# Optimization experiments

Measured on AMD Instinct MI355X. Metric: run time of the kernel, lower is better.

## Reference

```python
import jax, jax.numpy as jnp
import numpy as np

O, EI, EQ = 1024, 512, 512      # output_size, embedding_img, embedding_q
DI, DQ = 2048, 300              # input_img, input_q
LI, LQ = 1024, 32               # video frames, question length
V, T = 32000, 20                # vocab, decode steps


def _lstm_scan(x, Wi, Wh, b):
    # x: [L, D]; torch LSTM gate order i, f, g, o
    xp = x @ Wi.T  # [L, 4H] precompute input projection
    H = Wh.shape[1]
    def step(carry, xt):
        h, c = carry
        g = xt + Wh @ h + b
        i, f, gg, o = jnp.split(g, 4)
        c = jax.nn.sigmoid(f) * c + jax.nn.sigmoid(i) * jnp.tanh(gg)
        h = jax.nn.sigmoid(o) * jnp.tanh(c)
        return (h, c), h
    z = jnp.zeros((H,), x.dtype)
    _, hs = jax.lax.scan(step, (z, z), xp)
    return hs  # [L, H]


def _bilstm(x, Wif, Whf, bf, Wib, Whb, bb):
    hf = _lstm_scan(x, Wif, Whf, bf)
    hb = _lstm_scan(x[::-1], Wib, Whb, bb)[::-1]
    return jnp.concatenate([hf, hb], axis=-1)  # [L, 2H]


def _forward(img_feats, q_feats, Wi_imgf, Wh_imgf, b_imgf, Wi_imgb, Wh_imgb, b_imgb, Wi_qf, Wh_qf, b_qf, Wi_qb, Wh_qb, b_qb, Wimg_h, Wimg_e, bimg, Wq_h, Wq_e, bq, Wmod, bmod, Wmod_img, Wmod_q, Wfus_img, Wfus_q, Wfus, bfus, Wi_dec, Wh_dec, b_dec, Wfin, bfin, t_dec):
    img_emb = _bilstm(img_feats, Wi_imgf, Wh_imgf, b_imgf, Wi_imgb, Wh_imgb, b_imgb)  # [LI, 2EI]
    q_emb = _bilstm(q_feats, Wi_qf, Wh_qf, b_qf, Wi_qb, Wh_qb, b_qb)                  # [LQ, 2EQ]
    # static (encoder) part of the Bahdanau score: Linear(O+2E,1) split into h-part and e-part
    e_img = img_emb @ Wimg_e + bimg  # [LI]
    e_q = q_emb @ Wq_e + bq          # [LQ]

    def dec_step(carry, _):
        h, c = carry  # decoder hidden/cell, [O]
        # per-frame / per-word attention (h contribution is a constant shift under softmax)
        a_img = jax.nn.softmax(jnp.dot(Wimg_h, h) + e_img)
        a_q = jax.nn.softmax(jnp.dot(Wq_h, h) + e_q)
        ctx_img = a_img @ img_emb  # [2EI]
        ctx_q = a_q @ q_emb        # [2EQ]
        # modality-level attention
        tmp = jnp.dot(Wmod, h) + bmod
        wi = jnp.tanh(tmp + jnp.dot(Wmod_img, ctx_img))
        wq = jnp.tanh(tmp + jnp.dot(Wmod_q, ctx_q))
        mw = jax.nn.softmax(jnp.stack([wi, wq]))  # [2]
        d_img = Wfus_img @ ctx_img  # [O]
        d_q = Wfus_q @ ctx_q        # [O]
        fs = jnp.tanh(Wfus @ h + bfus + mw[0] * d_img + mw[1] * d_q)  # gated fusion, [O]
        # single-step decoder LSTM
        g = Wi_dec @ fs + Wh_dec @ h + b_dec
        i, f, gg, o = jnp.split(g, 4)
        c = jax.nn.sigmoid(f) * c + jax.nn.sigmoid(i) * jnp.tanh(gg)
        h = jax.nn.sigmoid(o) * jnp.tanh(c)
        logits = Wfin @ h + bfin  # [V]
        return (h, c), logits

    z = jnp.zeros((O,), img_feats.dtype)
    _, logits = jax.lax.scan(dec_step, (z, z), None, length=t_dec)
    return logits  # [T, V]


def setup_inputs() -> dict:
    ks = jax.random.split(jax.random.key(0), 40)
    def n(k, shape, s=0.05):
        return jax.random.normal(k, shape, dtype=jnp.float32) * s
    inp = {
        "img_feats": n(ks[0], (LI, DI), 1.0),
        "q_feats": n(ks[1], (LQ, DQ), 1.0),
        "Wi_imgf": n(ks[2], (4 * EI, DI)),
        "Wh_imgf": n(ks[3], (4 * EI, EI)),
        "b_imgf": n(ks[4], (4 * EI,)),
        "Wi_imgb": n(ks[5], (4 * EI, DI)),
        "Wh_imgb": n(ks[6], (4 * EI, EI)),
        "b_imgb": n(ks[7], (4 * EI,)),
        "Wi_qf": n(ks[8], (4 * EQ, DQ)),
        "Wh_qf": n(ks[9], (4 * EQ, EQ)),
        "b_qf": n(ks[10], (4 * EQ,)),
        "Wi_qb": n(ks[11], (4 * EQ, DQ)),
        "Wh_qb": n(ks[12], (4 * EQ, EQ)),
        "b_qb": n(ks[13], (4 * EQ,)),
        "Wimg_h": n(ks[14], (O,)),
        "Wimg_e": n(ks[15], (2 * EI,)),
        "bimg": n(ks[16], ()),
        "Wq_h": n(ks[17], (O,)),
        "Wq_e": n(ks[18], (2 * EQ,)),
        "bq": n(ks[19], ()),
        "Wmod": n(ks[20], (O,)),
        "bmod": n(ks[21], ()),
        "Wmod_img": n(ks[22], (2 * EI,)),
        "Wmod_q": n(ks[23], (2 * EQ,)),
        "Wfus_img": n(ks[24], (O, 2 * EI)),
        "Wfus_q": n(ks[25], (O, 2 * EQ)),
        "Wfus": n(ks[26], (O, O)),
        "bfus": n(ks[27], (O,)),
        "Wi_dec": n(ks[28], (4 * O, O)),
        "Wh_dec": n(ks[29], (4 * O, O)),
        "b_dec": n(ks[30], (4 * O,)),
        "Wfin": n(ks[31], (V, O)),
        "bfin": n(ks[32], (V,)),
        "t_dec": T,
    }
    return inp


def reference(img_feats, q_feats, Wi_imgf, Wh_imgf, b_imgf, Wi_imgb, Wh_imgb, b_imgb, Wi_qf, Wh_qf, b_qf, Wi_qb, Wh_qb, b_qb, Wimg_h, Wimg_e, bimg, Wq_h, Wq_e, bq, Wmod, bmod, Wmod_img, Wmod_q, Wfus_img, Wfus_q, Wfus, bfus, Wi_dec, Wh_dec, b_dec, Wfin, bfin, t_dec):
    return _forward(img_feats, q_feats, Wi_imgf, Wh_imgf, b_imgf, Wi_imgb, Wh_imgb, b_imgb, Wi_qf, Wh_qf, b_qf, Wi_qb, Wh_qb, b_qb, Wimg_h, Wimg_e, bimg, Wq_h, Wq_e, bq, Wmod, bmod, Wmod_img, Wmod_q, Wfus_img, Wfus_q, Wfus, bfus, Wi_dec, Wh_dec, b_dec, Wfin, bfin, t_dec)
```

## Files before the change

### kernel.cpp

```cpp
#include <hip/hip_runtime.h>
#include <hip/hip_bf16.h>

typedef unsigned int  u32;
typedef unsigned short u16;
typedef unsigned long long u64;
typedef float f32x4 __attribute__((ext_vector_type(4)));
typedef short bf16x8 __attribute__((ext_vector_type(8)));
typedef u32 u32x4 __attribute__((ext_vector_type(4)));

#define AGENT __HIP_MEMORY_SCOPE_AGENT
__device__ inline float aloadf(const float* p){ return __hip_atomic_load(p, __ATOMIC_RELAXED, AGENT); }
__device__ inline void  astoref(float* p, float v){ __hip_atomic_store(p, v, __ATOMIC_RELAXED, AGENT); }
__device__ inline int   aloadi(const int* p){ return __hip_atomic_load(p, __ATOMIC_RELAXED, AGENT); }
__device__ inline void  astorei_rel(int* p, int v){ __hip_atomic_store(p, v, __ATOMIC_RELEASE, AGENT); }

__device__ __host__ inline u16 f2bf(float f){
  u32 u = __builtin_bit_cast(u32, f);
  u += 0x7fffu + ((u >> 16) & 1u);
  return (u16)(u >> 16);
}
__device__ inline float bflo(u32 a){ return __uint_as_float(a << 16); }
__device__ inline float bfhi(u32 a){ return __uint_as_float(a & 0xffff0000u); }

__device__ inline float sigm(float x){
  return __builtin_amdgcn_rcpf(1.f + __expf(-x));
}
__device__ inline float ftanh(float x){
  float xc = fminf(fmaxf(x, -15.f), 15.f);
  float e = __expf(2.f * xc);
  return (e - 1.f) * __builtin_amdgcn_rcpf(e + 1.f);
}

__device__ inline u32x4 poll4(const u32* addr, u32 want){
  u32x4 w;
  do {
    asm volatile("global_load_dwordx4 %0, %1, off sc0 sc1\n\ts_waitcnt vmcnt(0)"
                 : "=&v"(w) : "v"(addr) : "memory");
  } while ((w.x >> 16) != want || (w.y >> 16) != want ||
           (w.z >> 16) != want || (w.w >> 16) != want);
  return w;
}
__device__ inline void store4(u32* addr, u32x4 q){
  asm volatile("global_store_dwordx4 %0, %1, off sc0 sc1"
               :: "v"(addr), "v"(q) : "memory");
}

__device__ inline float wred_sum(float v){
#pragma unroll
  for (int m = 32; m >= 1; m >>= 1) v += __shfl_xor(v, m, 64);
  return v;
}
__device__ inline float bred_sum(float v, float* red, int tid){
  v = wred_sum(v);
  if ((tid & 63) == 0) red[tid >> 6] = v;
  __syncthreads();
  float r = red[0] + red[1] + red[2] + red[3];
  __syncthreads();
  return r;
}
__device__ inline float bred_max(float v, float* red, int tid){
#pragma unroll
  for (int m = 32; m >= 1; m >>= 1) v = fmaxf(v, __shfl_xor(v, m, 64));
  if ((tid & 63) == 0) red[tid >> 6] = v;
  __syncthreads();
  float r = fmaxf(fmaxf(red[0], red[1]), fmaxf(red[2], red[3]));
  __syncthreads();
  return r;
}

__device__ inline float dot1024(const u16* __restrict__ row, const float* h, int lane){
  float s = 0.f;
#pragma unroll
  for (int c = 0; c < 4; ++c){
    int e = 4 * lane + 256 * c;
    uint2 a = *(const uint2*)(row + e);
    float4 x = *(const float4*)(h + e);
    s = fmaf(bflo(a.x), x.x, s); s = fmaf(bfhi(a.x), x.y, s);
    s = fmaf(bflo(a.y), x.z, s); s = fmaf(bfhi(a.y), x.w, s);
  }
  return s;
}

__device__ inline float4 dot4(const u16* __restrict__ W, size_t r, size_t rs,
                              const float* h, int lane){
  const u16* p0 = W + (r         ) * 1024;
  const u16* p1 = W + (r + rs    ) * 1024;
  const u16* p2 = W + (r + 2 * rs) * 1024;
  const u16* p3 = W + (r + 3 * rs) * 1024;
  float s0 = 0, s1 = 0, s2 = 0, s3 = 0;
#pragma unroll
  for (int c = 0; c < 4; ++c){
    int e = 4 * lane + 256 * c;
    float4 x = *(const float4*)(h + e);
    uint2 a0 = *(const uint2*)(p0 + e);
    uint2 a1 = *(const uint2*)(p1 + e);
    uint2 a2 = *(const uint2*)(p2 + e);
    uint2 a3 = *(const uint2*)(p3 + e);
    s0 = fmaf(bflo(a0.x), x.x, s0); s0 = fmaf(bfhi(a0.x), x.y, s0);
    s0 = fmaf(bflo(a0.y), x.z, s0); s0 = fmaf(bfhi(a0.y), x.w, s0);
    s1 = fmaf(bflo(a1.x), x.x, s1); s1 = fmaf(bfhi(a1.x), x.y, s1);
    s1 = fmaf(bflo(a1.y), x.z, s1); s1 = fmaf(bfhi(a1.y), x.w, s1);
    s2 = fmaf(bflo(a2.x), x.x, s2); s2 = fmaf(bfhi(a2.x), x.y, s2);
    s2 = fmaf(bflo(a2.y), x.z, s2); s2 = fmaf(bfhi(a2.y), x.w, s2);
    s3 = fmaf(bflo(a3.x), x.x, s3); s3 = fmaf(bfhi(a3.x), x.y, s3);
    s3 = fmaf(bflo(a3.y), x.z, s3); s3 = fmaf(bfhi(a3.y), x.w, s3);
  }
  s0 = wred_sum(s0); s1 = wred_sum(s1); s2 = wred_sum(s2); s3 = wred_sum(s3);
  return make_float4(s0, s1, s2, s3);
}

__global__ void k_cvt(const float* __restrict__ s, u16* __restrict__ d, int n4){
  int i = blockIdx.x * 256 + threadIdx.x;
  int stride = gridDim.x * 256;
  const float4* s4 = (const float4*)s;
  for (; i < n4; i += stride){
    float4 v = s4[i];
    ushort4 o;
    o.x = f2bf(v.x); o.y = f2bf(v.y); o.z = f2bf(v.z); o.w = f2bf(v.w);
    ((ushort4*)d)[i] = o;
  }
}

__global__ __launch_bounds__(256, 1) void k_gemm_xp(
    const u16* __restrict__ A,
    const u16* __restrict__ B0, const u16* __restrict__ B1,
    const float* __restrict__ bias0, const float* __restrict__ bias1,
    float* __restrict__ C0, float* __restrict__ C1)
{
  const int K = 2048, N = 2048;
  const int bx = blockIdx.x, by = blockIdx.y, z = blockIdx.z;
  const u16* B = z ? B1 : B0;
  const float* bias = z ? bias1 : bias0;
  float* C = z ? C1 : C0;
  const int tid = threadIdx.x;
  const int lane = tid & 63, wv = tid >> 6;
  const int m0 = by * 128, n0 = bx * 128;
  const int wm = (wv >> 1) * 64, wn = (wv & 1) * 64;

  __shared__ __align__(16) u16 lA[128 * 32];
  __shared__ __align__(16) u16 lB[128 * 32];

  f32x4 acc[4][4];
#pragma unroll
  for (int i = 0; i < 4; ++i)
#pragma unroll
    for (int j = 0; j < 4; ++j) acc[i][j] = (f32x4){0.f, 0.f, 0.f, 0.f};

  const int lrow = tid >> 2;
  const int lcol = (tid & 3) * 8;
  const u16* aBase = A + (size_t)(m0 + lrow) * K + lcol;
  const u16* bBase = B + (size_t)(n0 + lrow) * K + lcol;

  for (int kk = 0; kk < K; kk += 32){
#pragma unroll
    for (int io = 0; io < 2; ++io){
      __builtin_amdgcn_global_load_lds(
        (const __attribute__((address_space(1))) void*)(aBase + (size_t)io * 64 * K + kk),
        (__attribute__((address_space(3))) void*)((char*)lA + wv * 1024 + io * 4096), 16, 0, 0);
      __builtin_amdgcn_global_load_lds(
        (const __attribute__((address_space(1))) void*)(bBase + (size_t)io * 64 * K + kk),
        (__attribute__((address_space(3))) void*)((char*)lB + wv * 1024 + io * 4096), 16, 0, 0);
    }
    asm volatile("s_waitcnt vmcnt(0)");
    __syncthreads();

    bf16x8 af[4], bfr[4];
#pragma unroll
    for (int i = 0; i < 4; ++i){
      af[i]  = *(const bf16x8*)&lA[(wm + i * 16 + (lane & 15)) * 32 + (lane >> 4) * 8];
      bfr[i] = *(const bf16x8*)&lB[(wn + i * 16 + (lane & 15)) * 32 + (lane >> 4) * 8];
    }
#pragma unroll
    for (int i = 0; i < 4; ++i)
#pragma unroll
      for (int j = 0; j < 4; ++j)
        acc[i][j] = __builtin_amdgcn_mfma_f32_16x16x32_bf16(af[i], bfr[j], acc[i][j], 0, 0, 0);
    __syncthreads();
  }

  const int rbase = (lane >> 4) * 4;
  const int ccol = lane & 15;
#pragma unroll
  for (int i = 0; i < 4; ++i)
#pragma unroll
    for (int j = 0; j < 4; ++j){
      int col = n0 + wn + j * 16 + ccol;
      float bv = bias[col];
#pragma unroll
      for (int r2 = 0; r2 < 4; ++r2){
        int row = m0 + wm + i * 16 + rbase + r2;
        C[(size_t)row * N + col] = acc[i][j][r2] + bv;
      }
    }
}

__global__ __launch_bounds__(256, 1) void k_qxp(
    const float* __restrict__ qf,
    const float* __restrict__ W0, const float* __restrict__ W1,
    const float* __restrict__ bb0, const float* __restrict__ bb1,
    float* __restrict__ o0, float* __restrict__ o1)
{
  const int bx = blockIdx.x;
  const int z = blockIdx.y;
  const float* W = z ? W1 : W0;
  const float* bb = z ? bb1 : bb0;
  float* o = z ? o1 : o0;
  const int tid = threadIdx.x;
  __shared__ float xs[32 * 301];
  __shared__ float Ws[64 * 301];
  for (int idx = tid; idx < 32 * 300; idx += 256){
    int m = idx / 300, k = idx - m * 300;
    xs[m * 301 + k] = qf[idx];
  }
  for (int idx = tid; idx < 64 * 300; idx += 256){
    int j = idx / 300, k = idx - j * 300;
    Ws[j * 301 + k] = W[(size_t)(bx * 64 + j) * 300 + k];
  }
  __syncthreads();
  for (int i = 0; i < 8; ++i){
    int idx = tid + i * 256;
    int nl = idx >> 5, m = idx & 31;
    float s = 0;
    for (int k = 0; k < 300; ++k) s = fmaf(xs[m * 301 + k], Ws[nl * 301 + k], s);
    o[(size_t)m * 2048 + bx * 64 + nl] = s + bb[bx * 64 + nl];
  }
}

__global__ __launch_bounds__(256, 1) void k_scan(
    const float* __restrict__ WhA, const float* __restrict__ WhB,
    const float* __restrict__ WhC, const float* __restrict__ WhD,
    const float* __restrict__ xpA, const float* __restrict__ xpB,
    const float* __restrict__ xpC, const float* __restrict__ xpD,
    float* __restrict__ emb, float* __restrict__ embT,
    float* __restrict__ qemb, float* __restrict__ qembT,
    u32* hcomm )
{
  const int tid = threadIdx.x;
  const int dir = blockIdx.x >> 5;
  const int sub = blockIdx.x & 31;
  const float* Wh = dir == 0 ? WhA : dir == 1 ? WhB : dir == 2 ? WhC : WhD;
  const float* xp = dir == 0 ? xpA : dir == 1 ? xpB : dir == 2 ? xpC : xpD;
  const int L = (dir < 2) ? 1024 : 32;
  const int rev = dir & 1;
  float* oe  = (dir < 2) ? emb  : qemb;
  float* oeT = (dir < 2) ? embT : qembT;
  const int colbase = rev ? 512 : 0;
  const int eTL = (dir < 2) ? 1024 : 32;
  const int hbase = sub * 16;
  const int lane = tid & 63, wv = tid >> 6;
  const int g = tid >> 4;
  const int seg = tid & 15;
  const bool pub = (seg == 0);

  __shared__ float hl[512];

  int grows[4];
#pragma unroll
  for (int gate = 0; gate < 4; ++gate) grows[gate] = gate * 512 + hbase + g;

  u32 wpk0[16], wpk1[16], wpk2[16], wpk3[16];
  {
    const float2* r0 = (const float2*)(Wh + (size_t)grows[0] * 512) + seg;
    const float2* r1 = (const float2*)(Wh + (size_t)grows[1] * 512) + seg;
    const float2* r2 = (const float2*)(Wh + (size_t)grows[2] * 512) + seg;
    const float2* r3 = (const float2*)(Wh + (size_t)grows[3] * 512) + seg;
#pragma unroll
    for (int i = 0; i < 16; ++i){
      float2 a0 = r0[16 * i], a1 = r1[16 * i], a2 = r2[16 * i], a3 = r3[16 * i];
      wpk0[i] = (u32)f2bf(a0.x) | ((u32)f2bf(a0.y) << 16);
      wpk1[i] = (u32)f2bf(a1.x) | ((u32)f2bf(a1.y) << 16);
      wpk2[i] = (u32)f2bf(a2.x) | ((u32)f2bf(a2.y) << 16);
      wpk3[i] = (u32)f2bf(a3.x) | ((u32)f2bf(a3.y) << 16);
    }
  }

  float creg = 0.f;
  float xpv[4] = {0.f, 0.f, 0.f, 0.f};
  if (pub){
    int t0 = rev ? (L - 1) : 0;
#pragma unroll
    for (int gate = 0; gate < 4; ++gate) xpv[gate] = xp[(size_t)t0 * 2048 + grows[gate]];
  }

  u32* hcd = hcomm + dir * 1024;

  for (int t = 0; t < L; ++t){
    const u32 want = (u32)t;
    if (tid < 128){
      u32x4 w = poll4(hcd + ((t & 1) << 9) + 4 * tid, want);
      *(float4*)&hl[4 * tid] = make_float4(bflo(w.x), bflo(w.y), bflo(w.z), bflo(w.w));
    }
    __syncthreads();

    float2 hreg[16];
#pragma unroll
    for (int i = 0; i < 16; ++i) hreg[i] = *(const float2*)&hl[2 * (seg + 16 * i)];
    float s0 = 0, s1 = 0, s2 = 0, s3 = 0;
#pragma unroll
    for (int i = 0; i < 16; ++i){
      float hx = hreg[i].x, hy = hreg[i].y;
      s0 = fmaf(bflo(wpk0[i]), hx, s0); s0 = fmaf(bfhi(wpk0[i]), hy, s0);
      s1 = fmaf(bflo(wpk1[i]), hx, s1); s1 = fmaf(bfhi(wpk1[i]), hy, s1);
      s2 = fmaf(bflo(wpk2[i]), hx, s2); s2 = fmaf(bfhi(wpk2[i]), hy, s2);
      s3 = fmaf(bflo(wpk3[i]), hx, s3); s3 = fmaf(bfhi(wpk3[i]), hy, s3);
    }
#pragma unroll
    for (int m = 1; m < 16; m <<= 1){
      s0 += __shfl_xor(s0, m, 64); s1 += __shfl_xor(s1, m, 64);
      s2 += __shfl_xor(s2, m, 64); s3 += __shfl_xor(s3, m, 64);
    }
    u32 tg = 0;
    float hout = 0.f;
    if (pub){
      float gi = s0 + xpv[0], gf = s1 + xpv[1], gg = s2 + xpv[2], go = s3 + xpv[3];
      creg = sigm(gf) * creg + sigm(gi) * ftanh(gg);
      hout = sigm(go) * ftanh(creg);
      tg = ((u32)(t + 1) << 16) | (u32)f2bf(hout);
    }
    u32 q0 = __shfl(tg, 0), q1 = __shfl(tg, 16), q2 = __shfl(tg, 32), q3 = __shfl(tg, 48);
    if (lane == 0)
      store4(hcd + (((t + 1) & 1) << 9) + hbase + 4 * wv, (u32x4){q0, q1, q2, q3});
    if (pub){
      const int trow = rev ? (L - 1 - t) : t;
      int col = colbase + hbase + g;
      oe[(size_t)trow * 1024 + col] = hout;
      oeT[(size_t)col * eTL + trow] = hout;
      if (t + 1 < L){
        int tn = rev ? (L - 2 - t) : (t + 1);
#pragma unroll
        for (int gate = 0; gate < 4; ++gate) xpv[gate] = xp[(size_t)tn * 2048 + grows[gate]];
      }
    }
  }
}

#define DG 64
__device__ inline void dbar(int* st, int b, int pc, int tid){
  __syncthreads();
  if (tid == 0) astorei_rel(&st[b], pc);
  if (tid < DG){
    while (aloadi(&st[tid]) < pc) {}
  }
  __syncthreads();
}

struct DecArgs {
  const float *emb, *embT, *qemb, *qembT;
  const float *Wimg_e, *bimg, *Wmod_img;
  const float *Wq_e, *bq, *Wmod_q;
  const float *Wmod, *bmod;
  const u16 *Wfus_bf; const float *bfus;
  const u16 *WfusI_bf, *WfusQ_bf;
  const u16 *Wid_bf, *Whd_bf; const float *b_dec;
  float *e_img, *m_img, *e_q, *m_q;
  float *a_img, *a_q, *ctx_img, *ctx_q;
  float *d_img, *d_q, *scal;
  u32 *tfs, *thdec;
  float *hall;
  int *st; int T;
};

__global__ __launch_bounds__(256, 1) void k_dec(DecArgs A)
{
  const int b = blockIdx.x, tid = threadIdx.x;
  const int lane = tid & 63, wv = tid >> 6;
  __shared__ __align__(16) float hl[1024];
  __shared__ __align__(16) float fsl[1024];
  __shared__ float red[4];
  __shared__ float gb[4][16];
  __shared__ float cdec[16];
  __shared__ float aql[32];
  int pc = 0;

  {
#pragma unroll
    for (int rr = 0; rr < 4; ++rr){
      int l = b * 16 + wv * 4 + rr;
      const float* er = A.emb + (size_t)l * 1024;
      float se = 0, sm = 0;
#pragma unroll
      for (int i = 0; i < 16; ++i){
        int k = lane + (i << 6);
        float x = er[k];
        se = fmaf(x, A.Wimg_e[k], se);
        sm = fmaf(x, A.Wmod_img[k], sm);
      }
      se = wred_sum(se); sm = wred_sum(sm);
      if (lane == 0){ astoref(A.e_img + l, se + A.bimg[0]); astoref(A.m_img + l, sm); }
    }
    if (b < 32 && wv == 0){
      const float* qr = A.qemb + (size_t)b * 1024;
      float se2 = 0, sm2 = 0;
#pragma unroll
      for (int i = 0; i < 16; ++i){
        int k = lane + (i << 6);
        float x = qr[k];
        se2 = fmaf(x, A.Wq_e[k], se2);
        sm2 = fmaf(x, A.Wmod_q[k], sm2);
      }
      se2 = wred_sum(se2); sm2 = wred_sum(sm2);
      if (lane == 0){ astoref(A.e_q + b, se2 + A.bq[0]); astoref(A.m_q + b, sm2); }
    }
  }
  pc++; dbar(A.st, b, pc, tid);

  if (b == 0){
    for (int k = tid; k < 1024; k += 256){ fsl[k] = aloadf(A.e_img + k); hl[k] = aloadf(A.m_img + k); }
    __syncthreads();
    float lm = -3.4e38f;
    for (int k = tid; k < 1024; k += 256) lm = fmaxf(lm, fsl[k]);
    float M = bred_max(lm, red, tid);
    float ls = 0, lw = 0;
    for (int k = tid; k < 1024; k += 256){
      float e = expf(fsl[k] - M);
      fsl[k] = e; ls += e; lw += e * hl[k];
    }
    float S = bred_sum(ls, red, tid);
    float W = bred_sum(lw, red, tid);
    float inv = 1.f / S;
    for (int k = tid; k < 1024; k += 256) astoref(A.a_img + k, fsl[k] * inv);
    if (tid == 0) astoref(A.scal + 2, W * inv);
    if (tid < 64){
      float ev = (lane < 32) ? aloadf(A.e_q + lane) : -3.4e38f;
      float mv = (lane < 32) ? aloadf(A.m_q + lane) : 0.f;
      float M2 = ev;
#pragma unroll
      for (int m = 32; m >= 1; m >>= 1) M2 = fmaxf(M2, __shfl_xor(M2, m, 64));
      float e = (lane < 32) ? expf(ev - M2) : 0.f;
      float S2 = wred_sum(e);
      float W2 = wred_sum(e * mv);
      if (lane < 32) astoref(A.a_q + lane, e / S2);
      if (lane == 0) astoref(A.scal + 3, W2 / S2);
    }
  }
  pc++; dbar(A.st, b, pc, tid);

  {
    for (int k = tid; k < 1024; k += 256) hl[k] = aloadf(A.a_img + k);
    if (tid < 32) aql[tid] = aloadf(A.a_q + tid);
    __syncthreads();
#pragma unroll
    for (int cc = 0; cc < 4; ++cc){
      int c = b * 16 + wv * 4 + cc;
      const float* eT = A.embT + (size_t)c * 1024;
      float s = 0;
#pragma unroll
      for (int i = 0; i < 16; ++i){ int l = lane + (i << 6); s = fmaf(hl[l], eT[l], s); }
      s = wred_sum(s);
      if (lane == 0) astoref(A.ctx_img + c, s);
      const float* qT = A.qembT + (size_t)c * 32;
      float sq = (lane < 32) ? aql[lane] * qT[lane] : 0.f;
      sq = wred_sum(sq);
      if (lane == 0) astoref(A.ctx_q + c, sq);
    }
  }
  pc++; dbar(A.st, b, pc, tid);

  for (int k = tid; k < 1024; k += 256){ hl[k] = aloadf(A.ctx_img + k); fsl[k] = aloadf(A.ctx_q + k); }
  __syncthreads();
  {
    int r = b * 16 + wv * 4;
    float4 si = dot4(A.WfusI_bf, (size_t)r, 1, hl, lane);
    float4 sq = dot4(A.WfusQ_bf, (size_t)r, 1, fsl, lane);
    if (lane == 0){
      astoref(A.d_img + r + 0, si.x); astoref(A.d_q + r + 0, sq.x);
      astoref(A.d_img + r + 1, si.y); astoref(A.d_q + r + 1, sq.y);
      astoref(A.d_img + r + 2, si.z); astoref(A.d_q + r + 2, sq.z);
      astoref(A.d_img + r + 3, si.w); astoref(A.d_q + r + 3, sq.w);
    }
  }
  pc++; dbar(A.st, b, pc, tid);

  const int fr = b * 16 + wv * 4;
  float dimg_r[4], dq_r[4], bfus_r[4];
#pragma unroll
  for (int rr = 0; rr < 4; ++rr){
    dimg_r[rr] = aloadf(A.d_img + fr + rr);
    dq_r[rr]   = aloadf(A.d_q + fr + rr);
    bfus_r[rr] = A.bfus[fr + rr];
  }
  const float sc2 = aloadf(A.scal + 2), sc3 = aloadf(A.scal + 3);
  const float bmod0 = A.bmod[0];
  float wmod_r[4];
#pragma unroll
  for (int i = 0; i < 4; ++i) wmod_r[i] = A.Wmod[tid + (i << 8)];

  for (int k = tid; k < 1024; k += 256) hl[k] = 0.f;
  if (tid < 16) cdec[tid] = 0.f;
  __syncthreads();

  for (int t = 0; t < A.T; ++t){
    const u32 want = (u32)(t + 1);

    float part = 0;
#pragma unroll
    for (int i = 0; i < 4; ++i) part = fmaf(wmod_r[i], hl[tid + (i << 8)], part);
    float tmp = bred_sum(part, red, tid) + bmod0;
    float wi_ = ftanh(tmp + sc2), wq_ = ftanh(tmp + sc3);
    float mx = fmaxf(wi_, wq_);
    float e0 = __expf(wi_ - mx), e1 = __expf(wq_ - mx);
    float inv01 = __builtin_amdgcn_rcpf(e0 + e1);
    float mw0 = e0 * inv01, mw1 = e1 * inv01;

    {
      float4 sf = dot4(A.Wfus_bf, (size_t)fr, 1, hl, lane);
      if (lane == 0){
        float v0 = ftanh(sf.x + bfus_r[0] + mw0 * dimg_r[0] + mw1 * dq_r[0]);
        float v1 = ftanh(sf.y + bfus_r[1] + mw0 * dimg_r[1] + mw1 * dq_r[1]);
        float v2 = ftanh(sf.z + bfus_r[2] + mw0 * dimg_r[2] + mw1 * dq_r[2]);
        float v3 = ftanh(sf.w + bfus_r[3] + mw0 * dimg_r[3] + mw1 * dq_r[3]);
        u32x4 q = { (want << 16) | (u32)f2bf(v0), (want << 16) | (u32)f2bf(v1),
                    (want << 16) | (u32)f2bf(v2), (want << 16) | (u32)f2bf(v3) };
        store4(A.tfs + fr, q);
      }
    }

    {
      u32x4 w = poll4(A.tfs + 4 * tid, want);
      *(float4*)&fsl[4 * tid] = make_float4(bflo(w.x), bflo(w.y), bflo(w.z), bflo(w.w));
    }
    __syncthreads();

    {
      size_t g0 = (size_t)wv * 1024 + b * 16;
#pragma unroll
      for (int q4 = 0; q4 < 4; ++q4){
        float4 sa = dot4(A.Wid_bf, g0 + q4 * 4, 1, fsl, lane);
        float4 sb = dot4(A.Whd_bf, g0 + q4 * 4, 1, hl,  lane);
        if (lane == 0){
          gb[wv][q4 * 4 + 0] = sa.x + sb.x + A.b_dec[g0 + q4 * 4 + 0];
          gb[wv][q4 * 4 + 1] = sa.y + sb.y + A.b_dec[g0 + q4 * 4 + 1];
          gb[wv][q4 * 4 + 2] = sa.z + sb.z + A.b_dec[g0 + q4 * 4 + 2];
          gb[wv][q4 * 4 + 3] = sa.w + sb.w + A.b_dec[g0 + q4 * 4 + 3];
        }
      }
    }
    __syncthreads();
    u32 tg = 0;
    if (tid < 16){
      float gi = gb[0][tid], gf = gb[1][tid], gg = gb[2][tid], go = gb[3][tid];
      float c = sigm(gf) * cdec[tid] + sigm(gi) * ftanh(gg);
      cdec[tid] = c;
      float h = sigm(go) * ftanh(c);
      tg = (want << 16) | (u32)f2bf(h);
      A.hall[(size_t)t * 1024 + b * 16 + tid] = h;
    }
    if (wv == 0){
      u32 q0 = __shfl(tg, 4 * lane + 0), q1 = __shfl(tg, 4 * lane + 1);
      u32 q2 = __shfl(tg, 4 * lane + 2), q3 = __shfl(tg, 4 * lane + 3);
      if (lane < 4) store4(A.thdec + b * 16 + 4 * lane, (u32x4){q0, q1, q2, q3});
    }
    {
      u32x4 w = poll4(A.thdec + 4 * tid, want);
      *(float4*)&hl[4 * tid] = make_float4(bflo(w.x), bflo(w.y), bflo(w.z), bflo(w.w));
    }
    __syncthreads();
  }
}

__global__ __launch_bounds__(256, 1) void k_logits(
    const u16* __restrict__ Wfin, const float* __restrict__ bfin,
    const float* __restrict__ hall, float* __restrict__ out, int T)
{
  __shared__ u32 hp[20 * 512];
  const int tid = threadIdx.x;
  const int lane = tid & 63, wv = tid >> 6;
  const int n2 = T * 512;
  for (int idx = tid; idx < n2; idx += 256){
    float2 v = ((const float2*)hall)[idx];
    hp[idx] = (u32)f2bf(v.x) | ((u32)f2bf(v.y) << 16);
  }
  __syncthreads();
  const int gwv = blockIdx.x * 4 + wv;
#pragma unroll
  for (int gset = 0; gset < 4; ++gset){
    int r0 = gwv * 16 + gset * 4;
    uint2 wreg[4][4];
#pragma unroll
    for (int rr = 0; rr < 4; ++rr){
      const uint2* wr = (const uint2*)(Wfin + (size_t)(r0 + rr) * 1024);
#pragma unroll
      for (int c = 0; c < 4; ++c) wreg[rr][c] = wr[lane + 64 * c];
    }
    for (int t = 0; t < T; ++t){
      const uint2* hp2 = (const uint2*)&hp[t * 512];
      float s0 = 0, s1 = 0, s2 = 0, s3 = 0;
#pragma unroll
      for (int c = 0; c < 4; ++c){
        uint2 hw = hp2[lane + 64 * c];
        float h0 = bflo(hw.x), h1 = bfhi(hw.x), h2 = bflo(hw.y), h3 = bfhi(hw.y);
        uint2 a;
        a = wreg[0][c];
        s0 = fmaf(bflo(a.x), h0, s0); s0 = fmaf(bfhi(a.x), h1, s0);
        s0 = fmaf(bflo(a.y), h2, s0); s0 = fmaf(bfhi(a.y), h3, s0);
        a = wreg[1][c];
        s1 = fmaf(bflo(a.x), h0, s1); s1 = fmaf(bfhi(a.x), h1, s1);
        s1 = fmaf(bflo(a.y), h2, s1); s1 = fmaf(bfhi(a.y), h3, s1);
        a = wreg[2][c];
        s2 = fmaf(bflo(a.x), h0, s2); s2 = fmaf(bfhi(a.x), h1, s2);
        s2 = fmaf(bflo(a.y), h2, s2); s2 = fmaf(bfhi(a.y), h3, s2);
        a = wreg[3][c];
        s3 = fmaf(bflo(a.x), h0, s3); s3 = fmaf(bfhi(a.x), h1, s3);
        s3 = fmaf(bflo(a.y), h2, s3); s3 = fmaf(bfhi(a.y), h3, s3);
      }
      s0 = wred_sum(s0); s1 = wred_sum(s1); s2 = wred_sum(s2); s3 = wred_sum(s3);
      if (lane == 0){
        float* orow = out + (size_t)t * 32000;
        orow[r0 + 0] = s0 + bfin[r0 + 0];
        orow[r0 + 1] = s1 + bfin[r0 + 1];
        orow[r0 + 2] = s2 + bfin[r0 + 2];
        orow[r0 + 3] = s3 + bfin[r0 + 3];
      }
    }
  }
}

extern "C" void kernel_launch(void* const* d_in, const int* in_sizes, int n_in,
                              void* d_out, int out_size, void* d_ws, size_t ws_size,
                              hipStream_t stream)
{
  const float* img_feats = (const float*)d_in[0];
  const float* q_feats   = (const float*)d_in[1];
  const float* Wi_imgf = (const float*)d_in[2];
  const float* Wh_imgf = (const float*)d_in[3];
  const float* b_imgf  = (const float*)d_in[4];
  const float* Wi_imgb = (const float*)d_in[5];
  const float* Wh_imgb = (const float*)d_in[6];
  const float* b_imgb  = (const float*)d_in[7];
  const float* Wi_qf = (const float*)d_in[8];
  const float* Wh_qf = (const float*)d_in[9];
  const float* b_qf  = (const float*)d_in[10];
  const float* Wi_qb = (const float*)d_in[11];
  const float* Wh_qb = (const float*)d_in[12];
  const float* b_qb  = (const float*)d_in[13];
  const float* Wimg_e = (const float*)d_in[15];
  const float* bimg   = (const float*)d_in[16];
  const float* Wq_e   = (const float*)d_in[18];
  const float* bq     = (const float*)d_in[19];
  const float* Wmod   = (const float*)d_in[20];
  const float* bmod   = (const float*)d_in[21];
  const float* Wmod_img = (const float*)d_in[22];
  const float* Wmod_q   = (const float*)d_in[23];
  const float* Wfus_img = (const float*)d_in[24];
  const float* Wfus_q   = (const float*)d_in[25];
  const float* Wfus     = (const float*)d_in[26];
  const float* bfus     = (const float*)d_in[27];
  const float* Wi_dec = (const float*)d_in[28];
  const float* Wh_dec = (const float*)d_in[29];
  const float* b_dec  = (const float*)d_in[30];
  const float* Wfin = (const float*)d_in[31];
  const float* bfin = (const float*)d_in[32];
  const int T = out_size / 32000;

  char* ws = (char*)d_ws;
  size_t off = 0;
  auto alloc = [&](size_t bytes){ size_t o = off; off += (bytes + 255) & ~(size_t)255; return o; };
  const size_t oA    = alloc(1024ull * 2048 * 2);
  const size_t oWiF  = alloc(2048ull * 2048 * 2);
  const size_t oWiB  = alloc(2048ull * 2048 * 2);
  const size_t oWfin = alloc(32000ull * 1024 * 2);
  const size_t oWfu  = alloc(1024ull * 1024 * 2);
  const size_t oWfI  = alloc(1024ull * 1024 * 2);
  const size_t oWfQ  = alloc(1024ull * 1024 * 2);
  const size_t oWid  = alloc(4096ull * 1024 * 2);
  const size_t oWhd  = alloc(4096ull * 1024 * 2);
  const size_t oxpF  = alloc(1024ull * 2048 * 4);
  const size_t oxpB  = alloc(1024ull * 2048 * 4);
  const size_t oxpQF = alloc(32ull * 2048 * 4);
  const size_t oxpQB = alloc(32ull * 2048 * 4);
  const size_t oemb  = alloc(1024ull * 1024 * 4);
  const size_t oembT = alloc(1024ull * 1024 * 4);
  const size_t oqemb = alloc(32ull * 1024 * 4);
  const size_t oqembT= alloc(1024ull * 32 * 4);
  const size_t ohall = alloc(20ull * 1024 * 4);
  const size_t oeimg = alloc(1024 * 4);
  const size_t omimg = alloc(1024 * 4);
  const size_t oeq   = alloc(32 * 4);
  const size_t omq   = alloc(32 * 4);
  const size_t oaimg = alloc(1024 * 4);
  const size_t oaq   = alloc(32 * 4);
  const size_t octxi = alloc(1024 * 4);
  const size_t octxq = alloc(1024 * 4);
  const size_t odimg = alloc(1024 * 4);
  const size_t odq   = alloc(1024 * 4);
  const size_t oCTRL = off;
  const size_t ohcomm = alloc(4ull * 2 * 512 * 4);
  const size_t otfs   = alloc(1024 * 4);
  const size_t othdec = alloc(1024 * 4);
  const size_t odst   = alloc(64 * 4);
  const size_t oscal  = alloc(64 * 4);
  const size_t ctrlBytes = off - oCTRL;
  (void)ws_size; (void)n_in; (void)in_sizes;

  hipMemsetAsync(ws + oCTRL, 0, ctrlBytes, stream);

  auto cvt = [&](const float* s, size_t o, long n){
    int n4 = (int)(n >> 2);
    int g = (n4 + 255) / 256; if (g > 2048) g = 2048;
    k_cvt<<<dim3(g), dim3(256), 0, stream>>>(s, (u16*)(ws + o), n4);
  };
  cvt(img_feats, oA, 1024L * 2048);
  cvt(Wi_imgf, oWiF, 2048L * 2048);
  cvt(Wi_imgb, oWiB, 2048L * 2048);
  cvt(Wfin, oWfin, 32000L * 1024);
  cvt(Wfus, oWfu, 1024L * 1024);
  cvt(Wfus_img, oWfI, 1024L * 1024);
  cvt(Wfus_q, oWfQ, 1024L * 1024);
  cvt(Wi_dec, oWid, 4096L * 1024);
  cvt(Wh_dec, oWhd, 4096L * 1024);

  k_gemm_xp<<<dim3(16, 8, 2), dim3(256), 0, stream>>>(
      (const u16*)(ws + oA), (const u16*)(ws + oWiF), (const u16*)(ws + oWiB),
      b_imgf, b_imgb, (float*)(ws + oxpF), (float*)(ws + oxpB));

  k_qxp<<<dim3(32, 2), dim3(256), 0, stream>>>(
      q_feats, Wi_qf, Wi_qb, b_qf, b_qb,
      (float*)(ws + oxpQF), (float*)(ws + oxpQB));

  k_scan<<<dim3(128), dim3(256), 0, stream>>>(
      Wh_imgf, Wh_imgb, Wh_qf, Wh_qb,
      (const float*)(ws + oxpF), (const float*)(ws + oxpB),
      (const float*)(ws + oxpQF), (const float*)(ws + oxpQB),
      (float*)(ws + oemb), (float*)(ws + oembT),
      (float*)(ws + oqemb), (float*)(ws + oqembT),
      (u32*)(ws + ohcomm));

  DecArgs DA;
  DA.emb = (const float*)(ws + oemb); DA.embT = (const float*)(ws + oembT);
  DA.qemb = (const float*)(ws + oqemb); DA.qembT = (const float*)(ws + oqembT);
  DA.Wimg_e = Wimg_e; DA.bimg = bimg; DA.Wmod_img = Wmod_img;
  DA.Wq_e = Wq_e; DA.bq = bq; DA.Wmod_q = Wmod_q;
  DA.Wmod = Wmod; DA.bmod = bmod;
  DA.Wfus_bf = (const u16*)(ws + oWfu); DA.bfus = bfus;
  DA.WfusI_bf = (const u16*)(ws + oWfI); DA.WfusQ_bf = (const u16*)(ws + oWfQ);
  DA.Wid_bf = (const u16*)(ws + oWid); DA.Whd_bf = (const u16*)(ws + oWhd); DA.b_dec = b_dec;
  DA.e_img = (float*)(ws + oeimg); DA.m_img = (float*)(ws + omimg);
  DA.e_q = (float*)(ws + oeq); DA.m_q = (float*)(ws + omq);
  DA.a_img = (float*)(ws + oaimg); DA.a_q = (float*)(ws + oaq);
  DA.ctx_img = (float*)(ws + octxi); DA.ctx_q = (float*)(ws + octxq);
  DA.d_img = (float*)(ws + odimg); DA.d_q = (float*)(ws + odq);
  DA.scal = (float*)(ws + oscal);
  DA.tfs = (u32*)(ws + otfs); DA.thdec = (u32*)(ws + othdec);
  DA.hall = (float*)(ws + ohall);
  DA.st = (int*)(ws + odst); DA.T = T;

  k_dec<<<dim3(DG), dim3(256), 0, stream>>>(DA);

  k_logits<<<dim3(500), dim3(256), 0, stream>>>(
      (const u16*)(ws + oWfin), bfin, (const float*)(ws + ohall),
      (float*)d_out, T);
}
```

Baseline: 2.406 ms.

## Co-locate scan direction blocks per XCD and poll local-scope hidden-state copy first

The recurrent scan now launches 256 blocks and keeps only those whose index mod 8 is below 4. Blocks are assigned to XCDs round-robin, so each direction's 32 blocks likely share one XCD. Each step's hidden state is written twice, once with sc0 only (L2-local) and once with sc0 sc1 (device scope). Readers poll the local copy first, aiming to cut cross-die coherence latency on every step, and the h-buffer in LDS is double-buffered. Separately, the decoder issues its Wh·h dot products before waiting for the fused-input flag, overlapping that work with the wait. The design relies on an undocumented block-to-XCD mapping and adds extra stores per step.

```diff
diff --git a/kernel.cpp b/kernel.cpp
--- a/kernel.cpp
+++ b/kernel.cpp
@@ -40,8 +40,25 @@
            (w.z >> 16) != want || (w.w >> 16) != want);
   return w;
 }
+__device__ inline u32x4 poll4_dual(const u32* loc, const u32* glob, u32 want){
+  u32x4 w;
+  for (;;){
+    asm volatile("global_load_dwordx4 %0, %1, off sc0\n\ts_waitcnt vmcnt(0)"
+                 : "=&v"(w) : "v"(loc) : "memory");
+    if ((w.x >> 16) == want && (w.y >> 16) == want &&
+        (w.z >> 16) == want && (w.w >> 16) == want) return w;
+    asm volatile("global_load_dwordx4 %0, %1, off sc0 sc1\n\ts_waitcnt vmcnt(0)"
+                 : "=&v"(w) : "v"(glob) : "memory");
+    if ((w.x >> 16) == want && (w.y >> 16) == want &&
+        (w.z >> 16) == want && (w.w >> 16) == want) return w;
+  }
+}
 __device__ inline void store4(u32* addr, u32x4 q){
   asm volatile("global_store_dwordx4 %0, %1, off sc0 sc1"
+               :: "v"(addr), "v"(q) : "memory");
+}
+__device__ inline void store4_loc(u32* addr, u32x4 q){
+  asm volatile("global_store_dwordx4 %0, %1, off sc0"
                :: "v"(addr), "v"(q) : "memory");
 }
 
@@ -233,11 +250,14 @@
     const float* __restrict__ xpC, const float* __restrict__ xpD,
     float* __restrict__ emb, float* __restrict__ embT,
     float* __restrict__ qemb, float* __restrict__ qembT,
-    u32* hcomm )
+    u32* hcommL, u32* hcommG )
 {
+  const int b = blockIdx.x;
+  const int slot = b & 7;
+  if (slot >= 4) return;
+  const int dir = slot;
+  const int sub = b >> 3;
   const int tid = threadIdx.x;
-  const int dir = blockIdx.x >> 5;
-  const int sub = blockIdx.x & 31;
   const float* Wh = dir == 0 ? WhA : dir == 1 ? WhB : dir == 2 ? WhC : WhD;
   const float* xp = dir == 0 ? xpA : dir == 1 ? xpB : dir == 2 ? xpC : xpD;
   const int L = (dir < 2) ? 1024 : 32;
@@ -252,7 +272,7 @@
   const int seg = tid & 15;
   const bool pub = (seg == 0);
 
-  __shared__ float hl[512];
+  __shared__ float hl[2][512];
 
   int grows[4];
 #pragma unroll
@@ -282,19 +302,23 @@
     for (int gate = 0; gate < 4; ++gate) xpv[gate] = xp[(size_t)t0 * 2048 + grows[gate]];
   }
 
-  u32* hcd = hcomm + dir * 1024;
+  u32* hcl = hcommL + dir * 1024;
+  u32* hcg = hcommG + dir * 1024;
 
   for (int t = 0; t < L; ++t){
     const u32 want = (u32)t;
+    const int par = t & 1;
     if (tid < 128){
-      u32x4 w = poll4(hcd + ((t & 1) << 9) + 4 * tid, want);
-      *(float4*)&hl[4 * tid] = make_float4(bflo(w.x), bflo(w.y), bflo(w.z), bflo(w.w));
+      int o = (par << 9) + 4 * tid;
+      u32x4 w = poll4_dual(hcl + o, hcg + o, want);
+      *(float4*)&hl[par][4 * tid] =
+          make_float4(bflo(w.x), bflo(w.y), bflo(w.z), bflo(w.w));
     }
     __syncthreads();
 
     float2 hreg[16];
 #pragma unroll
-    for (int i = 0; i < 16; ++i) hreg[i] = *(const float2*)&hl[2 * (seg + 16 * i)];
+    for (int i = 0; i < 16; ++i) hreg[i] = *(const float2*)&hl[par][2 * (seg + 16 * i)];
     float s0 = 0, s1 = 0, s2 = 0, s3 = 0;
 #pragma unroll
     for (int i = 0; i < 16; ++i){
@@ -318,8 +342,12 @@
       tg = ((u32)(t + 1) << 16) | (u32)f2bf(hout);
     }
     u32 q0 = __shfl(tg, 0), q1 = __shfl(tg, 16), q2 = __shfl(tg, 32), q3 = __shfl(tg, 48);
-    if (lane == 0)
-      store4(hcd + (((t + 1) & 1) << 9) + hbase + 4 * wv, (u32x4){q0, q1, q2, q3});
+    if (lane == 0){
+      int o = (((t + 1) & 1) << 9) + hbase + 4 * wv;
+      u32x4 q = {q0, q1, q2, q3};
+      store4_loc(hcl + o, q);
+      store4(hcg + o, q);
+    }
     if (pub){
       const int trow = rev ? (L - 1 - t) : t;
       int col = colbase + hbase + g;
@@ -515,6 +543,12 @@
       }
     }
 
+    const size_t g0 = (size_t)wv * 1024 + b * 16;
+    float4 sbq[4];
+#pragma unroll
+    for (int q4 = 0; q4 < 4; ++q4)
+      sbq[q4] = dot4(A.Whd_bf, g0 + q4 * 4, 1, hl, lane);
+
     {
       u32x4 w = poll4(A.tfs + 4 * tid, want);
       *(float4*)&fsl[4 * tid] = make_float4(bflo(w.x), bflo(w.y), bflo(w.z), bflo(w.w));
@@ -522,16 +556,14 @@
     __syncthreads();
 
     {
-      size_t g0 = (size_t)wv * 1024 + b * 16;
 #pragma unroll
       for (int q4 = 0; q4 < 4; ++q4){
         float4 sa = dot4(A.Wid_bf, g0 + q4 * 4, 1, fsl, lane);
-        float4 sb = dot4(A.Whd_bf, g0 + q4 * 4, 1, hl,  lane);
         if (lane == 0){
-          gb[wv][q4 * 4 + 0] = sa.x + sb.x + A.b_dec[g0 + q4 * 4 + 0];
-          gb[wv][q4 * 4 + 1] = sa.y + sb.y + A.b_dec[g0 + q4 * 4 + 1];
-          gb[wv][q4 * 4 + 2] = sa.z + sb.z + A.b_dec[g0 + q4 * 4 + 2];
-          gb[wv][q4 * 4 + 3] = sa.w + sb.w + A.b_dec[g0 + q4 * 4 + 3];
+          gb[wv][q4 * 4 + 0] = sa.x + sbq[q4].x + A.b_dec[g0 + q4 * 4 + 0];
+          gb[wv][q4 * 4 + 1] = sa.y + sbq[q4].y + A.b_dec[g0 + q4 * 4 + 1];
+          gb[wv][q4 * 4 + 2] = sa.z + sbq[q4].z + A.b_dec[g0 + q4 * 4 + 2];
+          gb[wv][q4 * 4 + 3] = sa.w + sbq[q4].w + A.b_dec[g0 + q4 * 4 + 3];
         }
       }
     }
@@ -684,7 +716,8 @@
   const size_t odimg = alloc(1024 * 4);
   const size_t odq   = alloc(1024 * 4);
   const size_t oCTRL = off;
-  const size_t ohcomm = alloc(4ull * 2 * 512 * 4);
+  const size_t ohcommL = alloc(4ull * 2 * 512 * 4);
+  const size_t ohcommG = alloc(4ull * 2 * 512 * 4);
   const size_t otfs   = alloc(1024 * 4);
   const size_t othdec = alloc(1024 * 4);
   const size_t odst   = alloc(64 * 4);
@@ -717,13 +750,13 @@
       q_feats, Wi_qf, Wi_qb, b_qf, b_qb,
       (float*)(ws + oxpQF), (float*)(ws + oxpQB));
 
-  k_scan<<<dim3(128), dim3(256), 0, stream>>>(
+  k_scan<<<dim3(256), dim3(256), 0, stream>>>(
       Wh_imgf, Wh_imgb, Wh_qf, Wh_qb,
       (const float*)(ws + oxpF), (const float*)(ws + oxpB),
       (const float*)(ws + oxpQF), (const float*)(ws + oxpQB),
       (float*)(ws + oemb), (float*)(ws + oembT),
       (float*)(ws + oqemb), (float*)(ws + oqembT),
-      (u32*)(ws + ohcomm));
+      (u32*)(ws + ohcommL), (u32*)(ws + ohcommG));
 
   DecArgs DA;
   DA.emb = (const float*)(ws + oemb); DA.embT = (const float*)(ws + oembT);
```

After: 2.059 ms. 14.4% less time.
